# Kernel tuning notes

Measured on AMD Instinct MI355X. Metric: run time of the kernel, lower is better.

## Reference

```python
import jax, jax.numpy as jnp
import numpy as np

N = 500000      # total nodes
C = 256         # in_channels
H = 8           # num_heads
D = 32          # out_channels per head
G = 4096        # number of graphs in the batch


def setup_inputs() -> dict:
    key = jax.random.key(0)
    k1, k2, k3, k4, k5 = jax.random.split(key, 5)
    x = jax.random.normal(k1, (N, C), dtype=jnp.float32)
    batch = jnp.sort(jax.random.randint(k2, (N,), 0, G)).astype(jnp.int64)
    Wg = jax.random.normal(k3, (H, C), dtype=jnp.float32) / np.sqrt(C)
    Wn = jax.random.normal(k4, (H, C, D), dtype=jnp.float32) / np.sqrt(C)
    bn = jax.random.normal(k5, (H, D), dtype=jnp.float32) * 0.01
    return {"x": x, "batch": batch, "Wg": Wg, "Wn": Wn, "bn": bn}


def reference(x, batch, Wg, Wn, bn):
    batch = batch.astype(jnp.int32)
    # Gate logits for all heads at once: [N, H]
    gate = x @ Wg.T
    # Segment-wise (per-graph) stable softmax over nodes, per head
    m = jax.ops.segment_max(gate, batch, num_segments=G)        # [G, H]
    e = jnp.exp(gate - m[batch])                                # [N, H]
    s = jax.ops.segment_sum(e, batch, num_segments=G)           # [G, H]
    alpha = e / s[batch]                                        # [N, H]
    # Per-head value projection: [N, H, D]
    v = jnp.einsum('nc,hcd->nhd', x, Wn) + bn
    # Attention-weighted segment sum -> [G, H, D], concat heads -> [G, H*D]
    out = jax.ops.segment_sum(alpha[:, :, None] * v, batch, num_segments=G)
    return out.reshape(G, H * D)
```

## Files before the change

### kernel.cpp

```cpp
#include <hip/hip_runtime.h>
#include <hip/hip_bf16.h>
#include <cmath>

#define NN 500000
#define CC 256
#define HH 8
#define DD 32
#define GG 4096

typedef short bf16x8 __attribute__((ext_vector_type(8)));
typedef float f32x4 __attribute__((ext_vector_type(4)));

#define OFF_START 0
#define OFF_FLAG  16400

__device__ __forceinline__ int get_batch(const void* b, int i, int is64) {
    return is64 ? (int)((const long long*)b)[i] : ((const int*)b)[i];
}

__global__ void detect_kernel(const int* __restrict__ b32, int n, int* __restrict__ flag) {
    if (threadIdx.x == 0 && blockIdx.x == 0) {
        int a = b32[(n / 2) | 1];
        int b = b32[(n - 2) | 1];
        int c = b32[((n / 2) + (n / 4)) | 1];
        *flag = (a == 0 && b == 0 && c == 0) ? 1 : 0;
    }
}

__global__ void seg_offsets_kernel(const void* __restrict__ batch, const int* __restrict__ flag,
                                   int n, int g_total, int* __restrict__ start) {
    int is64 = *flag;
    int i = blockIdx.x * blockDim.x + threadIdx.x;
    if (i >= n) return;
    int b = get_batch(batch, i, is64);
    int prev = (i == 0) ? -1 : get_batch(batch, i - 1, is64);
    for (int g = prev + 1; g <= b; ++g) start[g] = i;
    if (i == n - 1) {
        for (int g = b + 1; g <= g_total; ++g) start[g] = n;
    }
}

__device__ __forceinline__ unsigned pack_bf2(float a, float b) {
    __hip_bfloat162 h2 = __float22bfloat162_rn(make_float2(a, b));
    unsigned u;
    __builtin_memcpy(&u, &h2, 4);
    return u;
}
__device__ __forceinline__ float ubf_lo(unsigned u) { return __uint_as_float(u << 16); }
__device__ __forceinline__ float ubf_hi(unsigned u) { return __uint_as_float(u & 0xffff0000u); }

__global__ __launch_bounds__(256, 4) void fused_kernel(const float* __restrict__ x,
                                                       const int* __restrict__ start,
                                                       const float* __restrict__ Wg,
                                                       const float* __restrict__ Wn,
                                                       const float* __restrict__ bn,
                                                       float* __restrict__ out) {
    __shared__ float4 xb4[2048];
    __shared__ uint4 e_q[64];
    __shared__ float red[32];
    __shared__ float inv_s[HH];

    int g = blockIdx.x, t = threadIdx.x;
    int s0 = start[g], s1 = start[g + 1], len = s1 - s0;

    if (len == 0) { out[(size_t)g * (HH * DD) + t] = 0.f; return; }

    const int w  = t >> 6;
    const int l  = t & 63;
    const int lr = l & 15;
    const int lk = l >> 4;

    bf16x8 wb[8];
    {
        int hc = lr & 7;
        const float4* wp4 = reinterpret_cast<const float4*>(Wg + hc * CC + lk * 8);
#pragma unroll
        for (int tt = 0; tt < 8; ++tt) {
            float4 wa = wp4[tt * 8], wbv = wp4[tt * 8 + 1];
            unsigned u01 = pack_bf2(wa.x, wa.y), u23 = pack_bf2(wa.z, wa.w);
            unsigned u45 = pack_bf2(wbv.x, wbv.y), u67 = pack_bf2(wbv.z, wbv.w);
            if (lr < 8) {
                wb[tt][0] = (short)(u01 & 0xffff); wb[tt][1] = (short)(u01 >> 16);
                wb[tt][2] = (short)(u23 & 0xffff); wb[tt][3] = (short)(u23 >> 16);
                wb[tt][4] = (short)(u45 & 0xffff); wb[tt][5] = (short)(u45 >> 16);
                wb[tt][6] = (short)(u67 & 0xffff); wb[tt][7] = (short)(u67 >> 16);
            } else {
#pragma unroll
                for (int j = 0; j < 8; ++j) wb[tt][j] = 0;
            }
        }
    }

    float acc[HH][4];
#pragma unroll
    for (int h = 0; h < HH; ++h)
#pragma unroll
        for (int e = 0; e < 4; ++e) acc[h][e] = 0.f;
    float s_part = 0.f;

    char* slice = (char*)xb4 + w * 8192;
    const float4* x4 = reinterpret_cast<const float4*>(x);
    const int sn = l >> 3, sub = l & 7;

    for (int tb = w * 16; tb < len; tb += 64) {
        int tl = (len - tb < 16) ? (len - tb) : 16;

#pragma unroll
        for (int pass = 0; pass < 2; ++pass) {
            int n = pass * 8 + sn;
            if (n < tl) {
                const float4* xr = x4 + (size_t)(s0 + tb + n) * (CC / 4) + sub;
                float4 v[8];
#pragma unroll
                for (int j = 0; j < 8; ++j) v[j] = xr[j * 8];
                char* rb = slice + n * 512;
                unsigned swz = (unsigned)((n & 7) << 4);
#pragma unroll
                for (int j = 0; j < 8; ++j) {
                    uint2 p;
                    p.x = pack_bf2(v[j].x, v[j].y);
                    p.y = pack_bf2(v[j].z, v[j].w);
                    *reinterpret_cast<uint2*>(rb + (((unsigned)((j * 8 + sub) * 8)) ^ swz)) = p;
                }
            }
        }

        f32x4 d = {0.f, 0.f, 0.f, 0.f};
        {
            char* rb = slice + lr * 512;
            unsigned swz = (unsigned)((lr & 7) << 4);
#pragma unroll
            for (int tt = 0; tt < 8; ++tt) {
                bf16x8 a = *reinterpret_cast<bf16x8*>(rb + (((unsigned)(lk * 16 + tt * 64)) ^ swz));
                d = __builtin_amdgcn_mfma_f32_16x16x32_bf16(a, wb[tt], d, 0, 0, 0);
            }
        }

        {
            unsigned short* ep = reinterpret_cast<unsigned short*>(e_q) + (w * 16) * 8;
#pragma unroll
            for (int r = 0; r < 4; ++r) {
                int n = lk * 4 + r;
                float e = 0.f;
                if (n < tl && lr < 8) { e = __expf(d[r]); s_part += e; }
                if (lr < 8) ep[n * 8 + lr] = (unsigned short)(pack_bf2(e, 0.f) & 0xffff);
            }
        }

        {
            const uint4* eq = e_q + w * 16;
            for (int i = 0; i < tl; ++i) {
                uint4 eu = eq[i];
                unsigned swz = (unsigned)((i & 7) << 4);
                uint2 xu = *reinterpret_cast<uint2*>(slice + i * 512 + (((unsigned)(l * 8)) ^ swz));
                float x0 = ubf_lo(xu.x), x1 = ubf_hi(xu.x);
                float x2 = ubf_lo(xu.y), x3 = ubf_hi(xu.y);
                float e0 = ubf_lo(eu.x), e1 = ubf_hi(eu.x);
                float e2 = ubf_lo(eu.y), e3 = ubf_hi(eu.y);
                float e4 = ubf_lo(eu.z), e5 = ubf_hi(eu.z);
                float e6 = ubf_lo(eu.w), e7 = ubf_hi(eu.w);
                acc[0][0] += e0 * x0; acc[0][1] += e0 * x1; acc[0][2] += e0 * x2; acc[0][3] += e0 * x3;
                acc[1][0] += e1 * x0; acc[1][1] += e1 * x1; acc[1][2] += e1 * x2; acc[1][3] += e1 * x3;
                acc[2][0] += e2 * x0; acc[2][1] += e2 * x1; acc[2][2] += e2 * x2; acc[2][3] += e2 * x3;
                acc[3][0] += e3 * x0; acc[3][1] += e3 * x1; acc[3][2] += e3 * x2; acc[3][3] += e3 * x3;
                acc[4][0] += e4 * x0; acc[4][1] += e4 * x1; acc[4][2] += e4 * x2; acc[4][3] += e4 * x3;
                acc[5][0] += e5 * x0; acc[5][1] += e5 * x1; acc[5][2] += e5 * x2; acc[5][3] += e5 * x3;
                acc[6][0] += e6 * x0; acc[6][1] += e6 * x1; acc[6][2] += e6 * x2; acc[6][3] += e6 * x3;
                acc[7][0] += e7 * x0; acc[7][1] += e7 * x1; acc[7][2] += e7 * x2; acc[7][3] += e7 * x3;
            }
        }
    }

    s_part += __shfl_xor(s_part, 16);
    s_part += __shfl_xor(s_part, 32);
    if (l < 8) red[w * 8 + l] = s_part;

#pragma unroll
    for (int h = 0; h < HH; ++h)
        xb4[w * 512 + h * 64 + l] = make_float4(acc[h][0], acc[h][1], acc[h][2], acc[h][3]);
    __syncthreads();

    if (t < HH) inv_s[t] = 1.f / (red[t] + red[8 + t] + red[16 + t] + red[24 + t]);

    float* xwf = reinterpret_cast<float*>(xb4);
    for (int idx = t; idx < HH * CC; idx += 256)
        xwf[idx] = xwf[idx] + xwf[2048 + idx] + xwf[4096 + idx] + xwf[6144 + idx];
    __syncthreads();

    int ph = t >> 5, pd = t & 31;
    const float* wnp = Wn + (size_t)ph * CC * DD + pd;
    float o = 0.f;
#pragma unroll 8
    for (int c0 = 0; c0 < CC; ++c0) {
        int ce = (c0 + 4 * ph) & 255;
        o += xwf[ph * 256 + ce] * wnp[(size_t)ce * DD];
    }
    o = bn[ph * DD + pd] + inv_s[ph] * o;
    out[(size_t)g * (HH * DD) + t] = o;
}

extern "C" void kernel_launch(void* const* d_in, const int* in_sizes, int n_in,
                              void* d_out, int out_size, void* d_ws, size_t ws_size,
                              hipStream_t stream) {
    const float* x     = (const float*)d_in[0];
    const void*  batch = d_in[1];
    const float* Wg    = (const float*)d_in[2];
    const float* Wn    = (const float*)d_in[3];
    const float* bn    = (const float*)d_in[4];
    float* out = (float*)d_out;

    char* w = (char*)d_ws;
    int* startp = (int*)(w + OFF_START);
    int* flag   = (int*)(w + OFF_FLAG);

    detect_kernel<<<1, 64, 0, stream>>>((const int*)batch, NN, flag);
    seg_offsets_kernel<<<(NN + 255) / 256, 256, 0, stream>>>(batch, flag, NN, GG, startp);
    fused_kernel<<<GG, 256, 0, stream>>>(x, startp, Wg, Wn, bn, out);
}
```

Before: 224.1 us.

## Prefetch next x tile into registers and shrink per-wave tile to eight nodes

Result: slower. 311.4 us (+39.0%).

```diff
diff --git a/kernel.cpp b/kernel.cpp
--- a/kernel.cpp
+++ b/kernel.cpp
@@ -56,7 +56,7 @@
                                                        const float* __restrict__ bn,
                                                        float* __restrict__ out) {
     __shared__ float4 xb4[2048];
-    __shared__ uint4 e_q[64];
+    __shared__ uint4 e_q[32];
     __shared__ float red[32];
     __shared__ float inv_s[HH];
 
@@ -69,6 +69,21 @@
     const int l  = t & 63;
     const int lr = l & 15;
     const int lk = l >> 4;
+    const int sn = l >> 3;
+    const int sub = l & 7;
+
+    const float4* x4 = reinterpret_cast<const float4*>(x);
+    char* slice = (char*)xb4 + w * 8192;
+
+    float4 pf[8];
+    {
+        int n = w * 8 + sn;
+        if (n < len) {
+            const float4* xr = x4 + (size_t)(s0 + n) * (CC / 4) + sub;
+#pragma unroll
+            for (int j = 0; j < 8; ++j) pf[j] = xr[j * 8];
+        }
+    }
 
     bf16x8 wb[8];
     {
@@ -98,37 +113,35 @@
         for (int e = 0; e < 4; ++e) acc[h][e] = 0.f;
     float s_part = 0.f;
 
-    char* slice = (char*)xb4 + w * 8192;
-    const float4* x4 = reinterpret_cast<const float4*>(x);
-    const int sn = l >> 3, sub = l & 7;
-
-    for (int tb = w * 16; tb < len; tb += 64) {
-        int tl = (len - tb < 16) ? (len - tb) : 16;
-
-#pragma unroll
-        for (int pass = 0; pass < 2; ++pass) {
-            int n = pass * 8 + sn;
-            if (n < tl) {
-                const float4* xr = x4 + (size_t)(s0 + tb + n) * (CC / 4) + sub;
-                float4 v[8];
-#pragma unroll
-                for (int j = 0; j < 8; ++j) v[j] = xr[j * 8];
-                char* rb = slice + n * 512;
-                unsigned swz = (unsigned)((n & 7) << 4);
-#pragma unroll
-                for (int j = 0; j < 8; ++j) {
-                    uint2 p;
-                    p.x = pack_bf2(v[j].x, v[j].y);
-                    p.y = pack_bf2(v[j].z, v[j].w);
-                    *reinterpret_cast<uint2*>(rb + (((unsigned)((j * 8 + sub) * 8)) ^ swz)) = p;
-                }
+    for (int tb = w * 8; tb < len; tb += 32) {
+        int tl = (len - tb < 8) ? (len - tb) : 8;
+
+        if (sn < tl) {
+            char* rb = slice + sn * 512;
+            unsigned swz = (unsigned)(sn << 4);
+#pragma unroll
+            for (int j = 0; j < 8; ++j) {
+                uint2 p;
+                p.x = pack_bf2(pf[j].x, pf[j].y);
+                p.y = pack_bf2(pf[j].z, pf[j].w);
+                *reinterpret_cast<uint2*>(rb + (((unsigned)((j * 8 + sub) * 8)) ^ swz)) = p;
+            }
+        }
+
+        {
+            int n = tb + 32 + sn;
+            if (n < len) {
+                const float4* xr = x4 + (size_t)(s0 + n) * (CC / 4) + sub;
+#pragma unroll
+                for (int j = 0; j < 8; ++j) pf[j] = xr[j * 8];
             }
         }
 
         f32x4 d = {0.f, 0.f, 0.f, 0.f};
         {
-            char* rb = slice + lr * 512;
-            unsigned swz = (unsigned)((lr & 7) << 4);
+            int ar = lr & 7;
+            char* rb = slice + ar * 512;
+            unsigned swz = (unsigned)(ar << 4);
 #pragma unroll
             for (int tt = 0; tt < 8; ++tt) {
                 bf16x8 a = *reinterpret_cast<bf16x8*>(rb + (((unsigned)(lk * 16 + tt * 64)) ^ swz));
@@ -137,18 +150,18 @@
         }
 
         {
-            unsigned short* ep = reinterpret_cast<unsigned short*>(e_q) + (w * 16) * 8;
+            unsigned short* ep = reinterpret_cast<unsigned short*>(e_q) + w * 64;
 #pragma unroll
             for (int r = 0; r < 4; ++r) {
                 int n = lk * 4 + r;
                 float e = 0.f;
                 if (n < tl && lr < 8) { e = __expf(d[r]); s_part += e; }
-                if (lr < 8) ep[n * 8 + lr] = (unsigned short)(pack_bf2(e, 0.f) & 0xffff);
-            }
-        }
-
-        {
-            const uint4* eq = e_q + w * 16;
+                if (n < 8 && lr < 8) ep[n * 8 + lr] = (unsigned short)(pack_bf2(e, 0.f) & 0xffff);
+            }
+        }
+
+        {
+            const uint4* eq = e_q + w * 8;
             for (int i = 0; i < tl; ++i) {
                 uint4 eu = eq[i];
                 unsigned swz = (unsigned)((i & 7) << 4);
```
